# Kernel optimization log

Hardware: AMD Instinct MI355X
Metric: run time of the kernel (lower is better)

Reference implementation:

```python
import jax, jax.numpy as jnp
import numpy as np

N, K, M, H, F = 4, 1024, 1024, 16, 4096
D = M // H  # per-head dim (dim_q = dim_v = 64)
EPS = 1e-5


def _mha(q_in, k_in, v_in, Wq, bq, Wk, bk, Wv, bv, Wo, bo, mask):
    # Wq/Wk/Wv: [H, M, D]; bq/bk/bv: [H, D]; Wo: [H*D, M]; bo: [M]
    q = jnp.einsum('nkm,hmd->nhkd', q_in, Wq) + bq[None, :, None, :]
    k = jnp.einsum('nkm,hmd->nhkd', k_in, Wk) + bk[None, :, None, :]
    v = jnp.einsum('nkm,hmd->nhkd', v_in, Wv) + bv[None, :, None, :]
    scores = jnp.einsum('nhkd,nhld->nhkl', q, k) / jnp.sqrt(jnp.asarray(D, q.dtype))
    if mask is not None:
        scores = jnp.where(mask[:, None, :, :] == 0, jnp.asarray(-jnp.inf, q.dtype), scores)
    attn = jax.nn.softmax(scores, axis=-1)          # [N,H,K,K]
    y = jnp.einsum('nhkl,nhld->nhkd', attn, v)      # [N,H,K,D]
    y = y.transpose(0, 2, 1, 3).reshape(q_in.shape[0], q_in.shape[1], -1)  # concat heads -> [N,K,H*D]
    return y @ Wo + bo


def _ln(x, g, b):
    mu = jnp.mean(x, axis=-1, keepdims=True)
    var = jnp.mean((x - mu) ** 2, axis=-1, keepdims=True)
    return (x - mu) * jax.lax.rsqrt(var + EPS) * g + b


def setup_inputs() -> dict:
    key = jax.random.key(0)
    ks = jax.random.split(key, 24)
    s = 0.02
    def rn(k, shape):
        return jax.random.normal(k, shape, dtype=jnp.float32) * s
    inp = {
        'dec_inp': jax.random.normal(ks[0], (N, K, M), dtype=jnp.float32),
        'enc_out': jax.random.normal(ks[1], (N, K, M), dtype=jnp.float32),
        'mask': jnp.tril(jnp.ones((K, K), dtype=jnp.int32))[None].repeat(N, axis=0),
        # self-attention params
        'Wq_s': rn(ks[2], (H, M, D)), 'bq_s': jnp.zeros((H, D)),
        'Wk_s': rn(ks[3], (H, M, D)), 'bk_s': jnp.zeros((H, D)),
        'Wv_s': rn(ks[4], (H, M, D)), 'bv_s': jnp.zeros((H, D)),
        'Wo_s': rn(ks[5], (H * D, M)), 'bo_s': jnp.zeros((M,)),
        # cross-attention params
        'Wq_c': rn(ks[6], (H, M, D)), 'bq_c': jnp.zeros((H, D)),
        'Wk_c': rn(ks[7], (H, M, D)), 'bk_c': jnp.zeros((H, D)),
        'Wv_c': rn(ks[8], (H, M, D)), 'bv_c': jnp.zeros((H, D)),
        'Wo_c': rn(ks[9], (H * D, M)), 'bo_c': jnp.zeros((M,)),
        # feedforward params
        'W1': rn(ks[10], (M, F)), 'b1': jnp.zeros((F,)),
        'W2': rn(ks[11], (F, M)), 'b2': jnp.zeros((M,)),
        # layernorm params
        'g1': jnp.ones((M,)), 'be1': jnp.zeros((M,)),
        'g2': jnp.ones((M,)), 'be2': jnp.zeros((M,)),
        'g3': jnp.ones((M,)), 'be3': jnp.zeros((M,)),
    }
    return inp


def reference(dec_inp, enc_out, mask,
              Wq_s, bq_s, Wk_s, bk_s, Wv_s, bv_s, Wo_s, bo_s,
              Wq_c, bq_c, Wk_c, bk_c, Wv_c, bv_c, Wo_c, bo_c,
              W1, b1, W2, b2, g1, be1, g2, be2, g3, be3):
    # masked self-attention + residual + LN (dropout = identity in eval)
    out1 = _mha(dec_inp, dec_inp, dec_inp, Wq_s, bq_s, Wk_s, bk_s, Wv_s, bv_s, Wo_s, bo_s, mask)
    out2 = _ln(dec_inp + out1, g1, be1)
    # cross-attention with encoder output + residual + LN
    out3 = _mha(out2, enc_out, enc_out, Wq_c, bq_c, Wk_c, bk_c, Wv_c, bv_c, Wo_c, bo_c, None)
    out4 = _ln(out3 + out2, g2, be2)
    # feedforward + residual + LN
    out5 = jax.nn.relu(out4 @ W1 + b1) @ W2 + b2
    return _ln(out5 + out4, g3, be3)
```

## Files before the change

### kernel.cpp

```cpp
#include <hip/hip_runtime.h>

#define NB   4
#define SEQ  1024
#define MD   1024
#define NH   16
#define HD   64
#define FF   4096
#define NK   (NB*SEQ)
#define EPSF 1e-5f
#define QS   3072

typedef short short8 __attribute__((ext_vector_type(8)));
typedef float f32x4  __attribute__((ext_vector_type(4)));
typedef unsigned short u16;
typedef unsigned int u32;

__device__ __forceinline__ u16 f2bf(float x) {
    union { float f; unsigned u; } v; v.f = x;
    unsigned r = v.u + 0x7FFF + ((v.u >> 16) & 1);
    return (u16)(r >> 16);
}
__device__ __forceinline__ u16 f2bf_trunc(float x) {
    union { float f; unsigned u; } v; v.f = x;
    return (u16)(v.u >> 16);
}
__device__ __forceinline__ float bf2f(u16 x) {
    union { unsigned u; float f; } v; v.u = ((unsigned)x) << 16;
    return v.f;
}
__device__ __forceinline__ void gload_lds16(const void* g, void* l) {
    __builtin_amdgcn_global_load_lds(
        (const __attribute__((address_space(1))) unsigned int*)g,
        (__attribute__((address_space(3))) unsigned int*)l,
        16, 0, 0);
}

__global__ __launch_bounds__(256) void conv_bf16(const float* __restrict__ s0,
                                                 const float* __restrict__ s1,
                                                 u16* __restrict__ d0,
                                                 u16* __restrict__ d1) {
    const float* S = blockIdx.y ? s1 : s0;
    u16* D = blockIdx.y ? d1 : d0;
    const int i = blockIdx.x * 256 + threadIdx.x;
    float4 v = ((const float4*)S)[i];
    ushort4 o;
    o.x = f2bf(v.x); o.y = f2bf(v.y); o.z = f2bf(v.z); o.w = f2bf(v.w);
    ((ushort4*)D)[i] = o;
}

__global__ __launch_bounds__(256) void mask_tiles(const int* __restrict__ mask,
                                                  int* __restrict__ cls,
                                                  u32* __restrict__ bits) {
    const int jt = blockIdx.x, qt = blockIdx.y, n = blockIdx.z;
    const int t = threadIdx.x;
    const int r = t >> 1, h2 = (t & 1) * 2;
    u32 bb[2];
#pragma unroll
    for (int sg = 0; sg < 2; ++sg) {
        const int* mp = &mask[((size_t)n * SEQ + qt * 128 + r) * SEQ + jt * 128 + (h2 + sg) * 32];
        u32 b = 0;
#pragma unroll
        for (int k = 0; k < 8; ++k) {
            int4 v = *(const int4*)(mp + k * 4);
            b |= (v.x ? 1u : 0u) << (k * 4 + 0);
            b |= (v.y ? 1u : 0u) << (k * 4 + 1);
            b |= (v.z ? 1u : 0u) << (k * 4 + 2);
            b |= (v.w ? 1u : 0u) << (k * 4 + 3);
        }
        bb[sg] = b;
    }
    const int tile = (n * 8 + qt) * 8 + jt;
    bits[((size_t)tile * 128 + r) * 4 + h2]     = bb[0];
    bits[((size_t)tile * 128 + r) * 4 + h2 + 1] = bb[1];
    const int nfull  = __syncthreads_count(bb[0] == 0xFFFFFFFFu && bb[1] == 0xFFFFFFFFu);
    const int nempty = __syncthreads_count(bb[0] == 0u && bb[1] == 0u);
    if (t == 0) cls[tile] = (nfull == 256) ? 2 : ((nempty == 256) ? 0 : 1);
}

struct QkvArgs { const float* src[6]; u16* dst[6]; };

__global__ __launch_bounds__(256) void repack_qkv(QkvArgs a) {
    const int m0 = blockIdx.x * 64;
    const int h  = blockIdx.y;
    const int w  = blockIdx.z;
    const float* W = a.src[w];
    u16* BT = a.dst[w];
    const int t = threadIdx.x;
    __shared__ u16 Ts[64][72];

    const int r = t >> 4, c4 = (t & 15) * 4;
#pragma unroll
    for (int p = 0; p < 4; ++p) {
        const int row = r + p * 16;
        float4 v = *(const float4*)&W[((size_t)h * 1024 + m0 + row) * 64 + c4];
        Ts[row][c4] = f2bf(v.x); Ts[row][c4 + 1] = f2bf(v.y);
        Ts[row][c4 + 2] = f2bf(v.z); Ts[row][c4 + 3] = f2bf(v.w);
    }
    __syncthreads();
    const int d = t >> 2, j0 = (t & 3) * 16;
#pragma unroll
    for (int p = 0; p < 4; ++p) {
        ushort4 o;
        o.x = Ts[j0 + p * 4 + 0][d]; o.y = Ts[j0 + p * 4 + 1][d];
        o.z = Ts[j0 + p * 4 + 2][d]; o.w = Ts[j0 + p * 4 + 3][d];
        *(ushort4*)&BT[((size_t)h * 64 + d) * 1024 + m0 + j0 + p * 4] = o;
    }
}

struct FD { const float* src; int ss; u16* dst; int ds; };
struct FlatArgs { FD d[10]; };

__global__ __launch_bounds__(256) void repack_flat(FlatArgs fa) {
    FD u = fa.d[blockIdx.z];
    const int r0 = blockIdx.x * 64;
    const int c0 = blockIdx.y * 64;
    const int t  = threadIdx.x;
    __shared__ u16 Ts[64][72];

    const int r = t >> 4, c4 = (t & 15) * 4;
#pragma unroll
    for (int p = 0; p < 4; ++p) {
        const int row = r + p * 16;
        float4 v = *(const float4*)&u.src[(size_t)(r0 + row) * u.ss + c0 + c4];
        Ts[row][c4] = f2bf(v.x); Ts[row][c4 + 1] = f2bf(v.y);
        Ts[row][c4 + 2] = f2bf(v.z); Ts[row][c4 + 3] = f2bf(v.w);
    }
    __syncthreads();
    const int d = t >> 2, j0 = (t & 3) * 16;
#pragma unroll
    for (int p = 0; p < 4; ++p) {
        ushort4 o;
        o.x = Ts[j0 + p * 4 + 0][d]; o.y = Ts[j0 + p * 4 + 1][d];
        o.z = Ts[j0 + p * 4 + 2][d]; o.w = Ts[j0 + p * 4 + 3][d];
        *(ushort4*)&u.dst[(size_t)(c0 + d) * u.ds + r0 + j0 + p * 4] = o;
    }
}

template<int OUT_BF16, int RELU, int RESID, int BIAS3, int PARTIAL, int VT>
__global__ __launch_bounds__(256) void gemm_mfma(const u16* __restrict__ A,
                                                 const u16* __restrict__ A2,
                                                 int Astride,
                                                 const u16* __restrict__ BT,
                                                 int Bstride,
                                                 const float* __restrict__ b0,
                                                 const float* __restrict__ b1p,
                                                 const float* __restrict__ b2p,
                                                 const float* __restrict__ resid,
                                                 void* __restrict__ Cout,
                                                 u16* __restrict__ VtOut,
                                                 int Kd, int Nd) {
    const int nt = blockIdx.x;
    const int mt = blockIdx.y;
    const int t  = threadIdx.x;
    const int wave = t >> 6, lane = t & 63;
    const int q = lane >> 4, l16 = lane & 15;
    const int wm = wave >> 1, wn = wave & 1;

    __shared__ __align__(16) u16 As[128 * 64];
    __shared__ __align__(16) u16 Bs[128 * 64];

    const int row0 = mt * 128, col0 = nt * 128;
    const u16* Ause = (col0 < 1024) ? A : A2;
    const int kBase = PARTIAL ? blockIdx.z * Kd : 0;

    f32x4 acc[4][4];
#pragma unroll
    for (int r = 0; r < 4; ++r)
#pragma unroll
        for (int c = 0; c < 4; ++c) acc[r][c] = (f32x4)0.0f;

    const int lrow = lane >> 3;
    const int lcb  = lane & 7;

    for (int k0 = 0; k0 < Kd; k0 += 64) {
        __syncthreads();
#pragma unroll
        for (int p = 0; p < 4; ++p) {
            const int rr = wave * 32 + p * 8 + lrow;
            const int gcb = lcb ^ (rr & 7);
            gload_lds16(Ause + (size_t)(row0 + rr) * Astride + kBase + k0 + gcb * 8, As + (size_t)(wave * 32 + p * 8) * 64);
            gload_lds16(BT   + (size_t)(col0 + rr) * Bstride + kBase + k0 + gcb * 8, Bs + (size_t)(wave * 32 + p * 8) * 64);
        }
        __syncthreads();

#pragma unroll
        for (int s = 0; s < 2; ++s) {
            const int pb = (q + s * 4) ^ (l16 & 7);
            short8 af[4], bf[4];
#pragma unroll
            for (int r = 0; r < 4; ++r)
                af[r] = *(const short8*)&As[(wm * 64 + r * 16 + l16) * 64 + pb * 8];
#pragma unroll
            for (int c = 0; c < 4; ++c)
                bf[c] = *(const short8*)&Bs[(wn * 64 + c * 16 + l16) * 64 + pb * 8];
#pragma unroll
            for (int r = 0; r < 4; ++r)
#pragma unroll
                for (int c = 0; c < 4; ++c)
                    acc[r][c] = __builtin_amdgcn_mfma_f32_16x16x32_bf16(af[r], bf[c], acc[r][c], 0, 0, 0);
        }
    }

    if (VT && col0 >= 2048) {
#pragma unroll
        for (int c = 0; c < 4; ++c) {
            const int col = col0 + wn * 64 + c * 16 + l16;
            const float bb = b2p[col & 1023];
            const int d = col & 63, hh = (col >> 6) & 15;
#pragma unroll
            for (int r = 0; r < 4; ++r) {
                const int row = row0 + wm * 64 + r * 16 + q * 4;
                const int nn = row >> 10, k = row & 1023;
                ushort4 o;
                o.x = f2bf(acc[r][c][0] + bb);
                o.y = f2bf(acc[r][c][1] + bb);
                o.z = f2bf(acc[r][c][2] + bb);
                o.w = f2bf(acc[r][c][3] + bb);
                *(ushort4*)&VtOut[((size_t)(nn * 16 + hh) * 64 + d) * 1024 + k] = o;
            }
        }
        return;
    }

    float* Pout = PARTIAL ? ((float*)Cout + (size_t)blockIdx.z * NK * Nd) : nullptr;

#pragma unroll
    for (int c = 0; c < 4; ++c) {
        const int col = col0 + wn * 64 + c * 16 + l16;
        float bb = 0.0f;
        if (!PARTIAL) {
            if (BIAS3) {
                const int sec = col >> 10;
                const float* bp = sec == 0 ? b0 : (sec == 1 ? b1p : b2p);
                bb = bp[col & 1023];
            } else {
                bb = b0[col];
            }
        }
#pragma unroll
        for (int r = 0; r < 4; ++r) {
#pragma unroll
            for (int reg = 0; reg < 4; ++reg) {
                const int row = row0 + wm * 64 + r * 16 + q * 4 + reg;
                float v = acc[r][c][reg] + bb;
                if (PARTIAL) {
                    Pout[(size_t)row * Nd + col] = acc[r][c][reg];
                } else {
                    if (RELU)  v = fmaxf(v, 0.0f);
                    if (RESID) v += resid[(size_t)row * Nd + col];
                    if (OUT_BF16) ((u16*)Cout)[(size_t)row * Nd + col] = f2bf(v);
                    else          ((float*)Cout)[(size_t)row * Nd + col] = v;
                }
            }
        }
    }
}

#define PSTR 136
#define ATTN_LDS (128*64*2 + 64*128*2 + 8*16*PSTR*2)

__global__ __launch_bounds__(512, 4) void attn_mfma(const u16* __restrict__ QKV,
                                                    const u16* __restrict__ Vt,
                                                    const int* __restrict__ cls,
                                                    const u32* __restrict__ bits,
                                                    u16* __restrict__ Yout) {
    const int qt = blockIdx.x;
    const int h  = blockIdx.y;
    const int n  = blockIdx.z;
    const int t  = threadIdx.x;
    const int wave = t >> 6;
    const int lane = t & 63;
    const int quad = lane >> 4;
    const int l16  = lane & 15;
    const int sw   = wave >> 2;
    const int wq   = wave & 3;

    extern __shared__ __align__(16) char smem[];
    u16* Ks = (u16*)smem;
    u16* Vs = (u16*)(smem + 128 * 64 * 2);
    u16* Pw = (u16*)(smem + 128 * 64 * 2 + 64 * 128 * 2) + wave * 16 * PSTR;

    const int bh = n * NH + h;
    const int i0 = qt * 128;

    int cl[8];
    if (cls) {
        const int* cp = &cls[(n * 8 + qt) * 8];
#pragma unroll
        for (int j = 0; j < 8; ++j) cl[j] = cp[j];
    } else {
#pragma unroll
        for (int j = 0; j < 8; ++j) cl[j] = 2;
    }

    short8 qf[2];
    {
        const u16* qrow = QKV + ((size_t)n * SEQ + i0 + sw * 64 + wq * 16 + l16) * QS + h * 64 + quad * 8;
        short8 a = *(const short8*)(qrow);
        short8 b = *(const short8*)(qrow + 32);
#pragma unroll
        for (int j = 0; j < 8; ++j) {
            qf[0][j] = (short)f2bf(bf2f((u16)a[j]) * 0.18033688f);
            qf[1][j] = (short)f2bf(bf2f((u16)b[j]) * 0.18033688f);
        }
    }

    f32x4 O[4];
#pragma unroll
    for (int d = 0; d < 4; ++d) O[d] = (f32x4)0.0f;
    float lrow[4] = {};

    const int krow = lane >> 3, kblk = lane & 7;
    const int vrow = lane >> 4, vblk = lane & 15;
    const int x7 = l16 & 7;

    for (int jt = 0; jt < SEQ / 128; ++jt) {
        const int c = cl[jt];
        if (c == 0) continue;
        __syncthreads();

#pragma unroll
        for (int p = 0; p < 2; ++p) {
            const int rr = wave * 16 + p * 8 + krow;
            const int kb = kblk ^ (rr & 7);
            gload_lds16(QKV + ((size_t)n * SEQ + jt * 128 + rr) * QS + 1024 + h * 64 + kb * 8,
                        Ks + (wave * 16 + p * 8) * 64);
        }
#pragma unroll
        for (int p = 0; p < 2; ++p) {
            const int rr = wave * 8 + p * 4 + vrow;
            const int kb = vblk ^ (rr & 15);
            gload_lds16(Vt + ((size_t)bh * HD + rr) * SEQ + jt * 128 + kb * 8,
                        Vs + (wave * 8 + p * 4) * 128);
        }
        __syncthreads();

        f32x4 S[8];
#pragma unroll
        for (int sub = 0; sub < 8; ++sub) {
            S[sub] = (f32x4)0.0f;
            const int row = sub * 16 + l16;
            short8 k0 = *(const short8*)&Ks[row * 64 + ((quad ^ x7) * 8)];
            S[sub] = __builtin_amdgcn_mfma_f32_16x16x32_bf16(qf[0], k0, S[sub], 0, 0, 0);
            short8 k1 = *(const short8*)&Ks[row * 64 + (((4 + quad) ^ x7) * 8)];
            S[sub] = __builtin_amdgcn_mfma_f32_16x16x32_bf16(qf[1], k1, S[sub], 0, 0, 0);
        }

        if (c == 1) {
#pragma unroll
            for (int reg = 0; reg < 4; ++reg) {
                const int row = sw * 64 + wq * 16 + quad * 4 + reg;
                const uint4 mm = *(const uint4*)&bits[((size_t)((n * 8 + qt) * 8 + jt) * 128 + row) * 4];
#pragma unroll
                for (int sub = 0; sub < 8; ++sub) {
                    const u32 seg = (sub >> 1) == 0 ? mm.x : (sub >> 1) == 1 ? mm.y : (sub >> 1) == 2 ? mm.z : mm.w;
                    if (!((seg >> ((sub & 1) * 16 + l16)) & 1u)) S[sub][reg] = -1e30f;
                }
            }
        }

#pragma unroll
        for (int reg = 0; reg < 4; ++reg) {
            float rs = 0.0f;
#pragma unroll
            for (int sub = 0; sub < 8; ++sub) {
                float e = exp2f(S[sub][reg]);
                Pw[(quad * 4 + reg) * PSTR + sub * 16 + l16] = f2bf_trunc(e);
                rs += e;
            }
            rs += __shfl_xor(rs, 1);
            rs += __shfl_xor(rs, 2);
            rs += __shfl_xor(rs, 4);
            rs += __shfl_xor(rs, 8);
            lrow[reg] += rs;
        }

        short8 pa[4];
#pragma unroll
        for (int ks = 0; ks < 4; ++ks)
            pa[ks] = *(const short8*)&Pw[l16 * PSTR + ks * 32 + quad * 8];
#pragma unroll
        for (int d = 0; d < 4; ++d) {
            const int row = d * 16 + l16;
#pragma unroll
            for (int ks = 0; ks < 4; ++ks) {
                short8 vb = *(const short8*)&Vs[row * 128 + (((ks * 4 + quad) ^ l16) & 15) * 8];
                O[d] = __builtin_amdgcn_mfma_f32_16x16x32_bf16(pa[ks], vb, O[d], 0, 0, 0);
            }
        }
    }

#pragma unroll
    for (int d = 0; d < 4; ++d) {
#pragma unroll
        for (int reg = 0; reg < 4; ++reg) {
            const int row = i0 + sw * 64 + wq * 16 + quad * 4 + reg;
            const int col = h * 64 + d * 16 + l16;
            Yout[((size_t)n * SEQ + row) * QS + col] = f2bf(O[d][reg] / lrow[reg]);
        }
    }
}

__global__ __launch_bounds__(256) void ln_kernel(const float* __restrict__ X,
                                                 const float* __restrict__ g,
                                                 const float* __restrict__ be,
                                                 float* __restrict__ Y,
                                                 u16* __restrict__ Yb) {
    const int row = blockIdx.x;
    const int t = threadIdx.x;
    __shared__ float red[256];

    const float4 v = ((const float4*)(X + (size_t)row * MD))[t];
    red[t] = v.x + v.y + v.z + v.w;
    __syncthreads();
    for (int s2 = 128; s2 > 0; s2 >>= 1) {
        if (t < s2) red[t] += red[t + s2];
        __syncthreads();
    }
    const float mu = red[0] * (1.0f / MD);
    __syncthreads();

    float dx = v.x - mu, dy = v.y - mu, dz = v.z - mu, dw = v.w - mu;
    red[t] = dx * dx + dy * dy + dz * dz + dw * dw;
    __syncthreads();
    for (int s2 = 128; s2 > 0; s2 >>= 1) {
        if (t < s2) red[t] += red[t + s2];
        __syncthreads();
    }
    const float var = red[0] * (1.0f / MD);
    const float rs = rsqrtf(var + EPSF);

    const float4 gv = ((const float4*)g)[t];
    const float4 bv = ((const float4*)be)[t];
    float4 o;
    o.x = dx * rs * gv.x + bv.x;
    o.y = dy * rs * gv.y + bv.y;
    o.z = dz * rs * gv.z + bv.z;
    o.w = dw * rs * gv.w + bv.w;
    if (Y) ((float4*)(Y + (size_t)row * MD))[t] = o;
    if (Yb) {
        ushort4 ob;
        ob.x = f2bf(o.x); ob.y = f2bf(o.y); ob.z = f2bf(o.z); ob.w = f2bf(o.w);
        ((ushort4*)(Yb + (size_t)row * MD))[t] = ob;
    }
}

__global__ __launch_bounds__(256) void ln_fused2(const float* __restrict__ p0,
                                                 const float* __restrict__ p1,
                                                 const float* __restrict__ bias,
                                                 const float* __restrict__ resid,
                                                 const float* __restrict__ g,
                                                 const float* __restrict__ be,
                                                 float* __restrict__ Y) {
    const int row = blockIdx.x;
    const int t = threadIdx.x;
    __shared__ float red[256];

    const float4 a = ((const float4*)(p0 + (size_t)row * MD))[t];
    const float4 b = ((const float4*)(p1 + (size_t)row * MD))[t];
    const float4 r = ((const float4*)(resid + (size_t)row * MD))[t];
    const float4 bi = ((const float4*)bias)[t];
    float4 v;
    v.x = a.x + b.x + r.x + bi.x;
    v.y = a.y + b.y + r.y + bi.y;
    v.z = a.z + b.z + r.z + bi.z;
    v.w = a.w + b.w + r.w + bi.w;

    red[t] = v.x + v.y + v.z + v.w;
    __syncthreads();
    for (int s2 = 128; s2 > 0; s2 >>= 1) {
        if (t < s2) red[t] += red[t + s2];
        __syncthreads();
    }
    const float mu = red[0] * (1.0f / MD);
    __syncthreads();

    float dx = v.x - mu, dy = v.y - mu, dz = v.z - mu, dw = v.w - mu;
    red[t] = dx * dx + dy * dy + dz * dz + dw * dw;
    __syncthreads();
    for (int s2 = 128; s2 > 0; s2 >>= 1) {
        if (t < s2) red[t] += red[t + s2];
        __syncthreads();
    }
    const float var = red[0] * (1.0f / MD);
    const float rs = rsqrtf(var + EPSF);

    const float4 gv = ((const float4*)g)[t];
    const float4 bv = ((const float4*)be)[t];
    float4 o;
    o.x = dx * rs * gv.x + bv.x;
    o.y = dy * rs * gv.y + bv.y;
    o.z = dz * rs * gv.z + bv.z;
    o.w = dw * rs * gv.w + bv.w;
    ((float4*)(Y + (size_t)row * MD))[t] = o;
}

extern "C" void kernel_launch(void* const* d_in, const int* in_sizes, int n_in,
                              void* d_out, int out_size, void* d_ws, size_t ws_size,
                              hipStream_t stream) {
    const float* dec  = (const float*)d_in[0];
    const float* enc  = (const float*)d_in[1];
    const int*   mask = (const int*)d_in[2];
    const float* Wq_s = (const float*)d_in[3];
    const float* bq_s = (const float*)d_in[4];
    const float* Wk_s = (const float*)d_in[5];
    const float* bk_s = (const float*)d_in[6];
    const float* Wv_s = (const float*)d_in[7];
    const float* bv_s = (const float*)d_in[8];
    const float* Wo_s = (const float*)d_in[9];
    const float* bo_s = (const float*)d_in[10];
    const float* Wq_c = (const float*)d_in[11];
    const float* bq_c = (const float*)d_in[12];
    const float* Wk_c = (const float*)d_in[13];
    const float* bk_c = (const float*)d_in[14];
    const float* Wv_c = (const float*)d_in[15];
    const float* bv_c = (const float*)d_in[16];
    const float* Wo_c = (const float*)d_in[17];
    const float* bo_c = (const float*)d_in[18];
    const float* W1   = (const float*)d_in[19];
    const float* b1   = (const float*)d_in[20];
    const float* W2   = (const float*)d_in[21];
    const float* b2   = (const float*)d_in[22];
    const float* g1   = (const float*)d_in[23];
    const float* be1  = (const float*)d_in[24];
    const float* g2   = (const float*)d_in[25];
    const float* be2  = (const float*)d_in[26];
    const float* g3   = (const float*)d_in[27];
    const float* be3  = (const float*)d_in[28];

    char* wsb = (char*)d_ws;
    const size_t MB = 1u << 20;
    u16*   decb  = (u16*)(wsb + 0 * MB);
    u16*   O2b   = (u16*)(wsb + 0 * MB);
    u16*   encb  = (u16*)(wsb + 8 * MB);
    u16*   O4b   = (u16*)(wsb + 8 * MB);
    u16*   WqkvsT= (u16*)(wsb + 16 * MB);
    u16*   WqkvcT= (u16*)(wsb + 22 * MB);
    u16*   WosT  = (u16*)(wsb + 28 * MB);
    u16*   WocT  = (u16*)(wsb + 30 * MB);
    u16*   W1T   = (u16*)(wsb + 32 * MB);
    u16*   W2T   = (u16*)(wsb + 40 * MB);
    u16*   QKVb  = (u16*)(wsb + 48 * MB);
    u16*   Vt    = (u16*)(wsb + 72 * MB);
    u16*   Hb    = (u16*)(wsb + 48 * MB);
    int*   mcls  = (int*)(wsb + 80 * MB);
    u32*   mbits = (u32*)(wsb + 80 * MB + 64 * 1024);
    float* Tb    = (float*)(wsb + 80 * MB);
    float* FP    = (float*)(wsb + 0 * MB);
    float* O2    = (float*)(wsb + 96 * MB);
    float* O4    = (float*)(wsb + 96 * MB);

    dim3 blk(256);
    dim3 blkA(512);
    dim3 gConv(NK * MD / 4 / 256, 2);
    dim3 gMask(8, 8, 4);
    dim3 gQkvW(16, 16, 6);
    dim3 gFlatW(16, 16, 10);
    dim3 gAttn(SEQ / 128, NH, NB);
    dim3 gQKV(QS / 128, NK / 128);
    dim3 gOut(MD / 128, NK / 128);
    dim3 gF1(FF / 128, NK / 128);
    dim3 gF2(MD / 128, NK / 128, 2);

    conv_bf16<<<gConv, blk, 0, stream>>>(dec, enc, decb, encb);
    mask_tiles<<<gMask, blk, 0, stream>>>(mask, mcls, mbits);

    QkvArgs qa;
    qa.src[0] = Wq_s; qa.src[1] = Wk_s; qa.src[2] = Wv_s;
    qa.src[3] = Wq_c; qa.src[4] = Wk_c; qa.src[5] = Wv_c;
    qa.dst[0] = WqkvsT;                 qa.dst[1] = WqkvsT + (size_t)1024 * 1024;
    qa.dst[2] = WqkvsT + (size_t)2048 * 1024;
    qa.dst[3] = WqkvcT;                 qa.dst[4] = WqkvcT + (size_t)1024 * 1024;
    qa.dst[5] = WqkvcT + (size_t)2048 * 1024;
    repack_qkv<<<gQkvW, blk, 0, stream>>>(qa);

    FlatArgs fa;
    fa.d[0] = { Wo_s, 1024, WosT, 1024 };
    fa.d[1] = { Wo_c, 1024, WocT, 1024 };
    for (int u = 0; u < 4; ++u)
        fa.d[2 + u] = { W1 + (size_t)u * 1024, 4096, W1T + (size_t)u * 1024 * 1024, 1024 };
    for (int u = 0; u < 4; ++u)
        fa.d[6 + u] = { W2 + (size_t)u * 1024 * 1024, 1024, W2T + (size_t)u * 1024, 4096 };
    repack_flat<<<gFlatW, blk, 0, stream>>>(fa);

    gemm_mfma<1, 0, 0, 1, 0, 1><<<gQKV, blk, 0, stream>>>(decb, decb, MD, WqkvsT, MD, bq_s, bk_s, bv_s, nullptr, QKVb, Vt, MD, QS);
    attn_mfma<<<gAttn, blkA, ATTN_LDS, stream>>>(QKVb, Vt, mcls, mbits, QKVb);
    gemm_mfma<0, 0, 1, 0, 0, 0><<<gOut, blk, 0, stream>>>(QKVb, QKVb, QS, WosT, MD, bo_s, nullptr, nullptr, dec, Tb, nullptr, MD, MD);
    ln_kernel<<<NK, blk, 0, stream>>>(Tb, g1, be1, O2, O2b);

    gemm_mfma<1, 0, 0, 1, 0, 1><<<gQKV, blk, 0, stream>>>(O2b, encb, MD, WqkvcT, MD, bq_c, bk_c, bv_c, nullptr, QKVb, Vt, MD, QS);
    attn_mfma<<<gAttn, blkA, ATTN_LDS, stream>>>(QKVb, Vt, nullptr, nullptr, QKVb);
    gemm_mfma<0, 0, 1, 0, 0, 0><<<gOut, blk, 0, stream>>>(QKVb, QKVb, QS, WocT, MD, bo_c, nullptr, nullptr, O2, Tb, nullptr, MD, MD);
    ln_kernel<<<NK, blk, 0, stream>>>(Tb, g2, be2, O4, O4b);

    gemm_mfma<1, 1, 0, 0, 0, 0><<<gF1, blk, 0, stream>>>(O4b, O4b, MD, W1T, MD, b1, nullptr, nullptr, nullptr, Hb, nullptr, MD, FF);
    gemm_mfma<0, 0, 0, 0, 1, 0><<<gF2, blk, 0, stream>>>(Hb, Hb, FF, W2T, FF, nullptr, nullptr, nullptr, nullptr, FP, nullptr, FF / 2, MD);
    ln_fused2<<<NK, blk, 0, stream>>>(FP, FP + (size_t)NK * MD, b2, O4, g3, be3, (float*)d_out);
}
```

Before: 375.4 us.

## Add 256x256-tile 512-thread GEMM kernel for QKV and FFN projections

Introduces a gemm256 kernel that computes 256x256 output tiles with 8 waves, each wave holding an 8x4 grid of 16x16 MFMA accumulators. It replaces the 128x128 gemm_mfma for the QKV, FF1 and FF2 GEMMs, and the V-transpose epilogue moves into the new kernel. The larger tile raises arithmetic intensity per LDS load and cuts redundant global reads of A and B. The cost is much smaller grids (192, 256 and 128 blocks), which can leave many of the MI355X's CUs idle. Each thread also carries twice the accumulator registers, and loads are still single-buffered.

```diff
diff --git a/kernel.cpp b/kernel.cpp
--- a/kernel.cpp
+++ b/kernel.cpp
@@ -201,27 +201,6 @@
         }
     }
 
-    if (VT && col0 >= 2048) {
-#pragma unroll
-        for (int c = 0; c < 4; ++c) {
-            const int col = col0 + wn * 64 + c * 16 + l16;
-            const float bb = b2p[col & 1023];
-            const int d = col & 63, hh = (col >> 6) & 15;
-#pragma unroll
-            for (int r = 0; r < 4; ++r) {
-                const int row = row0 + wm * 64 + r * 16 + q * 4;
-                const int nn = row >> 10, k = row & 1023;
-                ushort4 o;
-                o.x = f2bf(acc[r][c][0] + bb);
-                o.y = f2bf(acc[r][c][1] + bb);
-                o.z = f2bf(acc[r][c][2] + bb);
-                o.w = f2bf(acc[r][c][3] + bb);
-                *(ushort4*)&VtOut[((size_t)(nn * 16 + hh) * 64 + d) * 1024 + k] = o;
-            }
-        }
-        return;
-    }
-
     float* Pout = PARTIAL ? ((float*)Cout + (size_t)blockIdx.z * NK * Nd) : nullptr;
 
 #pragma unroll
@@ -248,6 +227,127 @@
                 } else {
                     if (RELU)  v = fmaxf(v, 0.0f);
                     if (RESID) v += resid[(size_t)row * Nd + col];
+                    if (OUT_BF16) ((u16*)Cout)[(size_t)row * Nd + col] = f2bf(v);
+                    else          ((float*)Cout)[(size_t)row * Nd + col] = v;
+                }
+            }
+        }
+    }
+}
+
+template<int OUT_BF16, int RELU, int BIAS3, int PARTIAL, int VT>
+__global__ __launch_bounds__(512, 2) void gemm256(const u16* __restrict__ A,
+                                                  const u16* __restrict__ A2,
+                                                  int Astride,
+                                                  const u16* __restrict__ BT,
+                                                  int Bstride,
+                                                  const float* __restrict__ b0,
+                                                  const float* __restrict__ b1p,
+                                                  const float* __restrict__ b2p,
+                                                  void* __restrict__ Cout,
+                                                  u16* __restrict__ VtOut,
+                                                  int Kd, int Nd) {
+    const int nt = blockIdx.x;
+    const int mt = blockIdx.y;
+    const int t  = threadIdx.x;
+    const int wave = t >> 6, lane = t & 63;
+    const int q = lane >> 4, l16 = lane & 15;
+    const int wm = wave >> 2, wn = wave & 3;
+
+    extern __shared__ __align__(16) char smem[];
+    u16* As = (u16*)smem;
+    u16* Bs = (u16*)(smem + 256 * 64 * 2);
+
+    const int row0 = mt * 256, col0 = nt * 256;
+    const u16* Ause = (col0 < 1024) ? A : A2;
+    const int kBase = PARTIAL ? blockIdx.z * Kd : 0;
+
+    f32x4 acc[8][4];
+#pragma unroll
+    for (int r = 0; r < 8; ++r)
+#pragma unroll
+        for (int c = 0; c < 4; ++c) acc[r][c] = (f32x4)0.0f;
+
+    const int lrow = lane >> 3;
+    const int lcb  = lane & 7;
+
+    for (int k0 = 0; k0 < Kd; k0 += 64) {
+        __syncthreads();
+#pragma unroll
+        for (int p = 0; p < 4; ++p) {
+            const int rr = wave * 32 + p * 8 + lrow;
+            const int gcb = lcb ^ (rr & 7);
+            gload_lds16(Ause + (size_t)(row0 + rr) * Astride + kBase + k0 + gcb * 8,
+                        As + (size_t)(wave * 32 + p * 8) * 64);
+            gload_lds16(BT   + (size_t)(col0 + rr) * Bstride + kBase + k0 + gcb * 8,
+                        Bs + (size_t)(wave * 32 + p * 8) * 64);
+        }
+        __syncthreads();
+
+#pragma unroll
+        for (int s = 0; s < 2; ++s) {
+            const int pb = (q + s * 4) ^ (l16 & 7);
+            short8 af[8], bf[4];
+#pragma unroll
+            for (int r = 0; r < 8; ++r)
+                af[r] = *(const short8*)&As[(wm * 128 + r * 16 + l16) * 64 + pb * 8];
+#pragma unroll
+            for (int c = 0; c < 4; ++c)
+                bf[c] = *(const short8*)&Bs[(wn * 64 + c * 16 + l16) * 64 + pb * 8];
+#pragma unroll
+            for (int r = 0; r < 8; ++r)
+#pragma unroll
+                for (int c = 0; c < 4; ++c)
+                    acc[r][c] = __builtin_amdgcn_mfma_f32_16x16x32_bf16(af[r], bf[c], acc[r][c], 0, 0, 0);
+        }
+    }
+
+    if (VT && col0 >= 2048) {
+#pragma unroll
+        for (int c = 0; c < 4; ++c) {
+            const int col = col0 + wn * 64 + c * 16 + l16;
+            const float bb = b2p[col & 1023];
+            const int d = col & 63, hh = (col >> 6) & 15;
+#pragma unroll
+            for (int r = 0; r < 8; ++r) {
+                const int row = row0 + wm * 128 + r * 16 + q * 4;
+                const int nn = row >> 10, k = row & 1023;
+                ushort4 o;
+                o.x = f2bf(acc[r][c][0] + bb);
+                o.y = f2bf(acc[r][c][1] + bb);
+                o.z = f2bf(acc[r][c][2] + bb);
+                o.w = f2bf(acc[r][c][3] + bb);
+                *(ushort4*)&VtOut[((size_t)(nn * 16 + hh) * 64 + d) * 1024 + k] = o;
+            }
+        }
+        return;
+    }
+
+    float* Pout = PARTIAL ? ((float*)Cout + (size_t)blockIdx.z * NK * Nd) : nullptr;
+
+#pragma unroll
+    for (int c = 0; c < 4; ++c) {
+        const int col = col0 + wn * 64 + c * 16 + l16;
+        float bb = 0.0f;
+        if (!PARTIAL) {
+            if (BIAS3) {
+                const int sec = col >> 10;
+                const float* bp = sec == 0 ? b0 : (sec == 1 ? b1p : b2p);
+                bb = bp[col & 1023];
+            } else {
+                bb = b0[col];
+            }
+        }
+#pragma unroll
+        for (int r = 0; r < 8; ++r) {
+#pragma unroll
+            for (int reg = 0; reg < 4; ++reg) {
+                const int row = row0 + wm * 128 + r * 16 + q * 4 + reg;
+                float v = acc[r][c][reg] + bb;
+                if (PARTIAL) {
+                    Pout[(size_t)row * Nd + col] = acc[r][c][reg];
+                } else {
+                    if (RELU)  v = fmaxf(v, 0.0f);
                     if (OUT_BF16) ((u16*)Cout)[(size_t)row * Nd + col] = f2bf(v);
                     else          ((float*)Cout)[(size_t)row * Nd + col] = v;
                 }
@@ -552,15 +652,17 @@
 
     dim3 blk(256);
     dim3 blkA(512);
+    dim3 blkG(512);
     dim3 gConv(NK * MD / 4 / 256, 2);
     dim3 gMask(8, 8, 4);
     dim3 gQkvW(16, 16, 6);
     dim3 gFlatW(16, 16, 10);
     dim3 gAttn(SEQ / 128, NH, NB);
-    dim3 gQKV(QS / 128, NK / 128);
+    dim3 gQKV(QS / 256, NK / 256);
     dim3 gOut(MD / 128, NK / 128);
-    dim3 gF1(FF / 128, NK / 128);
-    dim3 gF2(MD / 128, NK / 128, 2);
+    dim3 gF1(FF / 256, NK / 256);
+    dim3 gF2(MD / 256, NK / 256, 2);
+    const int G256_LDS = 256 * 64 * 2 * 2;
 
     conv_bf16<<<gConv, blk, 0, stream>>>(dec, enc, decb, encb);
     mask_tiles<<<gMask, blk, 0, stream>>>(mask, mcls, mbits);
@@ -583,17 +685,17 @@
         fa.d[6 + u] = { W2 + (size_t)u * 1024 * 1024, 1024, W2T + (size_t)u * 1024, 4096 };
     repack_flat<<<gFlatW, blk, 0, stream>>>(fa);
 
-    gemm_mfma<1, 0, 0, 1, 0, 1><<<gQKV, blk, 0, stream>>>(decb, decb, MD, WqkvsT, MD, bq_s, bk_s, bv_s, nullptr, QKVb, Vt, MD, QS);
+    gemm256<1, 0, 1, 0, 1><<<gQKV, blkG, G256_LDS, stream>>>(decb, decb, MD, WqkvsT, MD, bq_s, bk_s, bv_s, QKVb, Vt, MD, QS);
     attn_mfma<<<gAttn, blkA, ATTN_LDS, stream>>>(QKVb, Vt, mcls, mbits, QKVb);
     gemm_mfma<0, 0, 1, 0, 0, 0><<<gOut, blk, 0, stream>>>(QKVb, QKVb, QS, WosT, MD, bo_s, nullptr, nullptr, dec, Tb, nullptr, MD, MD);
     ln_kernel<<<NK, blk, 0, stream>>>(Tb, g1, be1, O2, O2b);
 
-    gemm_mfma<1, 0, 0, 1, 0, 1><<<gQKV, blk, 0, stream>>>(O2b, encb, MD, WqkvcT, MD, bq_c, bk_c, bv_c, nullptr, QKVb, Vt, MD, QS);
+    gemm256<1, 0, 1, 0, 1><<<gQKV, blkG, G256_LDS, stream>>>(O2b, encb, MD, WqkvcT, MD, bq_c, bk_c, bv_c, QKVb, Vt, MD, QS);
     attn_mfma<<<gAttn, blkA, ATTN_LDS, stream>>>(QKVb, Vt, nullptr, nullptr, QKVb);
     gemm_mfma<0, 0, 1, 0, 0, 0><<<gOut, blk, 0, stream>>>(QKVb, QKVb, QS, WocT, MD, bo_c, nullptr, nullptr, O2, Tb, nullptr, MD, MD);
     ln_kernel<<<NK, blk, 0, stream>>>(Tb, g2, be2, O4, O4b);
 
-    gemm_mfma<1, 1, 0, 0, 0, 0><<<gF1, blk, 0, stream>>>(O4b, O4b, MD, W1T, MD, b1, nullptr, nullptr, nullptr, Hb, nullptr, MD, FF);
-    gemm_mfma<0, 0, 0, 0, 1, 0><<<gF2, blk, 0, stream>>>(Hb, Hb, FF, W2T, FF, nullptr, nullptr, nullptr, nullptr, FP, nullptr, FF / 2, MD);
+    gemm256<1, 1, 0, 0, 0><<<gF1, blkG, G256_LDS, stream>>>(O4b, O4b, MD, W1T, MD, b1, nullptr, nullptr, Hb, nullptr, MD, FF);
+    gemm256<0, 0, 0, 1, 0><<<gF2, blkG, G256_LDS, stream>>>(Hb, Hb, FF, W2T, FF, nullptr, nullptr, nullptr, FP, nullptr, FF / 2, MD);
     ln_fused2<<<NK, blk, 0, stream>>>(FP, FP + (size_t)NK * MD, b2, O4, g3, be3, (float*)d_out);
 }
```

After: 403.6 us. 1.07x slower.
